# Kernel optimization log

Hardware: AMD Instinct MI355X
Metric: run time of the kernel (lower is better)

The kernel has to match this reference:

```python
import jax, jax.numpy as jnp
import numpy as np

EPS = 1e-5

def _ln(z, g, b):
    # LayerNorm over last axis (per the gammas/betas of shape (2, 3H))
    mu = jnp.mean(z, axis=-1, keepdims=True)
    var = jnp.var(z, axis=-1, keepdims=True)
    return g * (z - mu) * jax.lax.rsqrt(var + EPS) + b

def setup_inputs() -> dict:
    key = jax.random.key(0)
    ks = jax.random.split(key, 12)
    B, L, D_IN, H, A, DEPTH = 64, 512, 256, 256, 128, 4
    glorot = lambda k, sh: jax.random.normal(k, sh, jnp.float32) * np.sqrt(2.0 / (sh[0] + sh[1])).astype(np.float32)
    # variable-length prefix masks (bucketing/masking semantics of the layer)
    lengths = jax.random.randint(ks[0], (B, 1), L // 2, L + 1)
    mask = jnp.arange(L)[None, :] < lengths
    return {
        'x': jax.random.normal(ks[1], (B, L, D_IN), jnp.float32),
        'mask': mask,
        'W_emb': glorot(ks[2], (D_IN, H)),
        'b_emb': jnp.zeros((H,), jnp.float32),
        'W': glorot(ks[3], (H, 3 * H)),
        'U': glorot(ks[4], (H, 3 * H)),
        'b': jnp.zeros((3 * H,), jnp.float32),
        'W_action_1': glorot(ks[5], (H, A)),
        'U_action_1': glorot(ks[6], (H, A)),
        'b_action_1': jnp.zeros((A,), jnp.float32),
        'W_action_2': glorot(ks[7], (A, 2)),
        'b_action_2': jnp.zeros((2,), jnp.float32),
        'gammas': jnp.ones((2, 3 * H), jnp.float32),
        'betas': jnp.zeros((2, 3 * H), jnp.float32),
        'depth': DEPTH,
    }

def _run_depth(x_seq, m_seq, W, U, b, Wa1, Ua1, ba1, Wa2, ba2, gammas, betas):
    # x_seq: (L,B,H), m_seq: (L,B) bool
    H = W.shape[0]
    B = x_seq.shape[1]
    # precompute + layernorm the input projection for all steps (fusable)
    xp_all = _ln(jnp.einsum('lbh,hk->lbk', x_seq, W), gammas[0], betas[0])  # (L,B,3H)

    def step(h, inputs):
        xp, xt, mt = inputs  # (B,3H), (B,H), (B,)
        hp = _ln(h @ U, gammas[1], betas[1])
        r = jax.nn.sigmoid(xp[:, :H] + hp[:, :H] + b[:H])
        z = jax.nn.sigmoid(xp[:, H:2 * H] + hp[:, H:2 * H] + b[H:2 * H])
        hh = jnp.tanh(xp[:, 2 * H:] + r * hp[:, 2 * H:] + b[2 * H:])
        h_new = z * h + (1.0 - z) * hh
        # action-policy subnetwork (binary merge/propagate decision)
        logits = jnp.tanh(xt @ Wa1 + h @ Ua1 + ba1) @ Wa2 + ba2  # (B,2)
        pol = jax.nn.softmax(logits, axis=-1)
        act = (pol[:, 1] > pol[:, 0]) & mt
        h_out = jnp.where(mt[:, None], h_new, h)  # masked steps carry state
        return h_out, (h_out, act, pol)

    h0 = jnp.zeros((B, H), x_seq.dtype)
    _, (h_seq, act_seq, pol_seq) = jax.lax.scan(step, h0, (xp_all, x_seq, m_seq))
    return h_seq, act_seq, pol_seq

def reference(x, mask, W_emb, b_emb, W, U, b, W_action_1, U_action_1, b_action_1,
              W_action_2, b_action_2, gammas, betas, depth):
    # embedding projection, then time-major like the Theano scans
    h_seq = jnp.swapaxes(x @ W_emb + b_emb, 0, 1)  # (L,B,H)
    m_seq = jnp.swapaxes(mask, 0, 1)               # (L,B)
    actions, policies = [], []
    for _ in range(depth):  # vertical (tree-depth) scan: small fixed count
        h_new, act, pol = _run_depth(h_seq, m_seq, W, U, b,
                                     W_action_1, U_action_1, b_action_1,
                                     W_action_2, b_action_2, gammas, betas)
        actions.append(act)
        policies.append(pol)
        h_seq = h_new
        m_seq = m_seq & act  # tree collapse: only selected nodes survive upward
    output = h_seq[-1]  # (B,H) final hidden state of top layer
    action = jnp.stack(actions, 0).transpose(2, 0, 1)      # (B,depth,L)
    policy = jnp.stack(policies, 0).transpose(2, 0, 1, 3)  # (B,depth,L,2)
    return output, action, policy
```

## Files before the change

### kernel.cpp

```cpp
#include <hip/hip_runtime.h>
#include <hip/hip_bf16.h>
#include <math.h>

#define BB 64
#define LL 512
#define HH 256
#define H3 768
#define AA 128
#define NDEPTH 4
#define NROWS (LL*BB)

#define EXCH_U64_PER_CHAIN (2 * 3 * 256)

typedef float vf32x32 __attribute__((ext_vector_type(32)));

__global__ void maskcvt_kernel(const unsigned char* __restrict__ raw,
                               int* __restrict__ m)
{
    int i = blockIdx.x * blockDim.x + threadIdx.x;
    bool bytemode = (raw[1] == 1);
    int v;
    if (bytemode) v = raw[i] ? 1 : 0;
    else          v = (((const int*)raw)[i] != 0) ? 1 : 0;
    m[i] = v;
}

template<int MODE, int EPI>
__global__ __launch_bounds__(256) void gemm_kernel(
    const float* __restrict__ A, const float* __restrict__ Bm,
    const float* __restrict__ bias, const float* __restrict__ aux,
    float* __restrict__ C, int M, int N)
{
    __shared__ float As[16][136];
    __shared__ float Bs[16][136];
    const int tid = threadIdx.x;
    const int tx = tid & 15, ty = tid >> 4;
    const int row0 = blockIdx.y * 128, col0 = blockIdx.x * 128;

    float acc[8][8];
#pragma unroll
    for (int i = 0; i < 8; ++i)
#pragma unroll
        for (int j = 0; j < 8; ++j) acc[i][j] = 0.f;

    for (int kk = 0; kk < 256; kk += 16) {
#pragma unroll
        for (int i = 0; i < 2; ++i) {
            int aid = i * 256 + tid;
            int r   = aid >> 2;
            int k4  = (aid & 3) << 2;
            int rr  = row0 + r;
            float4 v;
            if (MODE == 0) {
                v = *(const float4*)(A + rr * 256 + kk + k4);
            } else if (MODE == 1) {
                v = *(const float4*)(A + (rr & 63) * 131072 + (rr >> 6) * 256 + kk + k4);
            } else {
                if (rr < 64) v = make_float4(0.f, 0.f, 0.f, 0.f);
                else         v = *(const float4*)(A + (rr - 64) * 256 + kk + k4);
            }
            As[k4 + 0][r] = v.x; As[k4 + 1][r] = v.y;
            As[k4 + 2][r] = v.z; As[k4 + 3][r] = v.w;

            int bid = i * 256 + tid;
            int bk  = bid >> 5;
            int c4  = (bid & 31) << 2;
            float4 w = *(const float4*)(Bm + (kk + bk) * N + col0 + c4);
            *(float4*)&Bs[bk][c4] = w;
        }
        __syncthreads();
#pragma unroll
        for (int k = 0; k < 16; ++k) {
            float a[8], bb2[8];
            *(float4*)&a[0]   = *(const float4*)&As[k][ty * 8];
            *(float4*)&a[4]   = *(const float4*)&As[k][ty * 8 + 4];
            *(float4*)&bb2[0] = *(const float4*)&Bs[k][tx * 8];
            *(float4*)&bb2[4] = *(const float4*)&Bs[k][tx * 8 + 4];
#pragma unroll
            for (int i = 0; i < 8; ++i)
#pragma unroll
                for (int j = 0; j < 8; ++j)
                    acc[i][j] += a[i] * bb2[j];
        }
        __syncthreads();
    }

#pragma unroll
    for (int i = 0; i < 8; ++i) {
        int row  = row0 + ty * 8 + i;
        int colb = col0 + tx * 8;
        float vout[8];
#pragma unroll
        for (int j = 0; j < 8; ++j) {
            float v = acc[i][j];
            if (EPI == 1) v += bias[colb + j];
            if (EPI == 2) v = tanhf(v + aux[row * N + colb + j]);
            vout[j] = v;
        }
        *(float4*)&C[row * N + colb]     = *(float4*)&vout[0];
        *(float4*)&C[row * N + colb + 4] = *(float4*)&vout[4];
    }
}

__global__ __launch_bounds__(256) void lnrows_kernel(
    float* __restrict__ XP, const float* __restrict__ g0,
    const float* __restrict__ b0, const float* __restrict__ gb)
{
    const int row = blockIdx.x;
    const int tid = threadIdx.x;
    float* p = XP + (long)row * H3;
    float v0 = p[tid], v1 = p[tid + 256], v2 = p[tid + 512];
    float s = v0 + v1 + v2;
    float q = v0 * v0 + v1 * v1 + v2 * v2;
#pragma unroll
    for (int off = 32; off >= 1; off >>= 1) {
        s += __shfl_xor(s, off);
        q += __shfl_xor(q, off);
    }
    __shared__ float rs4[4], rq4[4];
    if ((tid & 63) == 0) { rs4[tid >> 6] = s; rq4[tid >> 6] = q; }
    __syncthreads();
    float S = rs4[0] + rs4[1] + rs4[2] + rs4[3];
    float Q = rq4[0] + rq4[1] + rq4[2] + rq4[3];
    float mu  = S * (1.f / 768.f);
    float var = Q * (1.f / 768.f) - mu * mu;
    float r   = rsqrtf(var + 1e-5f);
    p[tid]       = g0[tid]       * (v0 - mu) * r + b0[tid]       + gb[tid];
    p[tid + 256] = g0[tid + 256] * (v1 - mu) * r + b0[tid + 256] + gb[tid + 256];
    p[tid + 512] = g0[tid + 512] * (v2 - mu) * r + b0[tid + 512] + gb[tid + 512];
}

__global__ __launch_bounds__(512, 2) void scan3_kernel(
    const float* __restrict__ XP,
    const float* __restrict__ U,
    const float* __restrict__ g1, const float* __restrict__ b1,
    const int* __restrict__ mask,
    float* __restrict__ Y,
    unsigned long long* __restrict__ exch,
    int seq0)
{
    const int i0   = blockIdx.x;
    const int xcd  = i0 & 7;
    const int slot = i0 >> 3;
    const int b    = xcd + 8 * (slot / 3);
    const int s    = slot % 3;
    const int tid  = threadIdx.x;
    const int kg   = tid >> 5;
    const int cg   = tid & 31;
    const int q1   = (s + 1 >= 3) ? s - 2 : s + 1;
    const int q2   = (s + 2 >= 3) ? s - 1 : s + 2;

    __shared__ float h_cur[256];
    __shared__ float part[16][256];
    __shared__ float xp_lds[768];
    __shared__ float g1s[768], b1s[768];
    __shared__ int   mk[512];
    __shared__ float reds[4], redq[4];

    vf32x32 u0v, u1v, u2v, u3v;
    {
        const volatile float* Uv = U;
        const int colbase = s * 256 + cg;
#pragma unroll
        for (int i = 0; i < 16; ++i) {
#pragma unroll
            for (int j = 0; j < 8; ++j) {
                const int f = i * 8 + j;
                float val = Uv[(kg * 16 + i) * H3 + colbase + 32 * j];
                if      (f < 32) u0v[f]      = val;
                else if (f < 64) u1v[f - 32] = val;
                else if (f < 96) u2v[f - 64] = val;
                else             u3v[f - 96] = val;
            }
        }
    }
    if (tid < 256) h_cur[tid] = 0.f;
    for (int i = tid; i < 768; i += 512) { g1s[i] = g1[i]; b1s[i] = b1[i]; }
    mk[tid] = mask[b * LL + tid];
    __syncthreads();

    unsigned long long* exb = exch + b * EXCH_U64_PER_CHAIN;
    int seq = seq0;

    for (int l = 0; l < LL; ++l) {
        if (!mk[l]) {
            if (s == 0 && tid < 64) {
                float4 hv = *(const float4*)&h_cur[tid * 4];
                *(float4*)&Y[((long)l * BB + b) * HH + tid * 4] = hv;
            }
            continue;
        }
        seq++;
        const int par = seq & 1;

        float4 xr4;
        if (tid < 192) xr4 = *(const float4*)(XP + ((long)l * BB + b) * H3 + tid * 4);

        float acc[8] = {0.f, 0.f, 0.f, 0.f, 0.f, 0.f, 0.f, 0.f};
#pragma unroll
        for (int i = 0; i < 4; ++i) {
            float4 hv = *(const float4*)&h_cur[kg * 16 + i * 4];
#pragma unroll
            for (int e = 0; e < 4; ++e) {
                const float hh = (e == 0) ? hv.x : (e == 1) ? hv.y
                               : (e == 2) ? hv.z : hv.w;
                const int ik = i * 4 + e;
#pragma unroll
                for (int j = 0; j < 8; ++j) {
                    const int f = ik * 8 + j;
                    const float uu = (f < 32) ? u0v[f]
                                   : (f < 64) ? u1v[f - 32]
                                   : (f < 96) ? u2v[f - 64]
                                   :            u3v[f - 96];
                    acc[j] += uu * hh;
                }
            }
        }
#pragma unroll
        for (int j = 0; j < 8; ++j)
            part[kg][cg + 32 * j] = acc[j];
        __syncthreads();

        if (tid < 192) *(float4*)&xp_lds[tid * 4] = xr4;

        float pre = 0.f, v0 = 0.f, v1 = 0.f, v2 = 0.f;
        if (tid < 256) {
            pre = part[0][tid];
#pragma unroll
            for (int gg = 1; gg < 16; ++gg) pre += part[gg][tid];

            unsigned long long pk =
                ((unsigned long long)(unsigned)seq << 32) |
                (unsigned long long)__float_as_uint(pre);
            __hip_atomic_store(&exb[(par * 3 + s) * 256 + tid], pk,
                               __ATOMIC_RELAXED, __HIP_MEMORY_SCOPE_AGENT);

            unsigned long long x1, x2;
            do {
                x1 = __hip_atomic_load(&exb[(par * 3 + q1) * 256 + tid],
                                       __ATOMIC_RELAXED, __HIP_MEMORY_SCOPE_AGENT);
            } while ((int)(x1 >> 32) != seq);
            do {
                x2 = __hip_atomic_load(&exb[(par * 3 + q2) * 256 + tid],
                                       __ATOMIC_RELAXED, __HIP_MEMORY_SCOPE_AGENT);
            } while ((int)(x2 >> 32) != seq);
            float w1 = __uint_as_float((unsigned)x1);
            float w2 = __uint_as_float((unsigned)x2);
            v0 = (s == 0) ? pre : ((q1 == 0) ? w1 : w2);
            v1 = (s == 1) ? pre : ((q1 == 1) ? w1 : w2);
            v2 = (s == 2) ? pre : ((q1 == 2) ? w1 : w2);

            float st = v0 + v1 + v2;
            float qt = v0 * v0 + v1 * v1 + v2 * v2;
#pragma unroll
            for (int off = 32; off >= 1; off >>= 1) {
                st += __shfl_xor(st, off);
                qt += __shfl_xor(qt, off);
            }
            if ((tid & 63) == 0) { reds[tid >> 6] = st; redq[tid >> 6] = qt; }
        }
        __syncthreads();

        if (tid < 256) {
            float S = reds[0] + reds[1] + reds[2] + reds[3];
            float Q = redq[0] + redq[1] + redq[2] + redq[3];
            float mu = S * (1.f / 768.f);
            float rs = rsqrtf(Q * (1.f / 768.f) - mu * mu + 1e-5f);
            float hp_r = g1s[tid]       * (v0 - mu) * rs + b1s[tid];
            float hp_z = g1s[256 + tid] * (v1 - mu) * rs + b1s[256 + tid];
            float hp_h = g1s[512 + tid] * (v2 - mu) * rs + b1s[512 + tid];
            float xr = xp_lds[tid], xz = xp_lds[256 + tid], xh = xp_lds[512 + tid];
            float r  = 1.f / (1.f + expf(-(xr + hp_r)));
            float z  = 1.f / (1.f + expf(-(xz + hp_z)));
            float hh = tanhf(xh + r * hp_h);
            float o  = z * h_cur[tid] + (1.f - z) * hh;
            h_cur[tid] = o;
            if (s == 0) Y[((long)l * BB + b) * HH + tid] = o;
        }
        __syncthreads();
    }
}

__global__ __launch_bounds__(256) void act_kernel(
    const float* __restrict__ T, const float* __restrict__ Wa2,
    const float* __restrict__ ba2, const int* __restrict__ mask_in,
    int* __restrict__ mask_out, float* __restrict__ act_out,
    float* __restrict__ pol_out, int d)
{
    int row  = blockIdx.x * 4 + (threadIdx.x >> 6);
    int lane = threadIdx.x & 63;
    const float* Tr = T + (long)row * AA;
    float t0 = Tr[lane], t1 = Tr[lane + 64];
    float l0 = t0 * Wa2[lane * 2]       + t1 * Wa2[(lane + 64) * 2];
    float l1 = t0 * Wa2[lane * 2 + 1]   + t1 * Wa2[(lane + 64) * 2 + 1];
#pragma unroll
    for (int off = 32; off >= 1; off >>= 1) {
        l0 += __shfl_xor(l0, off);
        l1 += __shfl_xor(l1, off);
    }
    if (lane == 0) {
        int l = row >> 6, bb = row & 63;
        l0 += ba2[0]; l1 += ba2[1];
        float m  = fmaxf(l0, l1);
        float e0 = expf(l0 - m), e1 = expf(l1 - m);
        float inv = 1.f / (e0 + e1);
        float p0 = e0 * inv, p1 = e1 * inv;
        int mt = mask_in[bb * LL + l];
        int a  = (p1 > p0) && mt;
        act_out[bb * (NDEPTH * LL) + d * LL + l] = a ? 1.f : 0.f;
        pol_out[bb * (NDEPTH * LL * 2) + d * (LL * 2) + l * 2 + 0] = p0;
        pol_out[bb * (NDEPTH * LL * 2) + d * (LL * 2) + l * 2 + 1] = p1;
        mask_out[bb * LL + l] = a;
    }
}

__global__ void final_copy_kernel(const float* __restrict__ X, float* __restrict__ out)
{
    int i = blockIdx.x * blockDim.x + threadIdx.x;
    int bb = i >> 8, j = i & 255;
    out[i] = X[((long)(LL - 1) * BB + bb) * HH + j];
}

extern "C" void kernel_launch(void* const* d_in, const int* in_sizes, int n_in,
                              void* d_out, int out_size, void* d_ws, size_t ws_size,
                              hipStream_t stream)
{
    const float* x      = (const float*)d_in[0];
    const void*  mraw   = d_in[1];
    const float* W_emb  = (const float*)d_in[2];
    const float* b_emb  = (const float*)d_in[3];
    const float* W      = (const float*)d_in[4];
    const float* U      = (const float*)d_in[5];
    const float* bias3  = (const float*)d_in[6];
    const float* Wa1    = (const float*)d_in[7];
    const float* Ua1    = (const float*)d_in[8];
    const float* ba1    = (const float*)d_in[9];
    const float* Wa2    = (const float*)d_in[10];
    const float* ba2    = (const float*)d_in[11];
    const float* gammas = (const float*)d_in[12];
    const float* betas  = (const float*)d_in[13];

    float* out = (float*)d_out;
    char*  ws  = (char*)d_ws;

    float* XP = (float*)(ws);
    float* X  = (float*)(ws + 100663296UL);
    float* Y  = (float*)(ws + 134217728UL);
    float* XA = (float*)(ws + 167772160UL);
    float* T  = XP;
    int*   m0 = (int*)(ws + 184549376UL);
    int*   m1 = (int*)(ws + 184680448UL);

    float* act_out = out + BB * HH;
    float* pol_out = act_out + BB * NDEPTH * LL;

    maskcvt_kernel<<<dim3(NROWS / 256), dim3(256), 0, stream>>>(
        (const unsigned char*)mraw, m0);

    gemm_kernel<1, 1><<<dim3(2, 256), dim3(256), 0, stream>>>(
        x, W_emb, b_emb, nullptr, X, NROWS, HH);

    float* Xc = X; float* Yc = Y;
    int* mc = m0; int* mn = m1;

    for (int d = 0; d < NDEPTH; ++d) {
        gemm_kernel<0, 0><<<dim3(6, 256), dim3(256), 0, stream>>>(
            Xc, W, nullptr, nullptr, XP, NROWS, H3);
        lnrows_kernel<<<dim3(NROWS), dim3(256), 0, stream>>>(
            XP, gammas, betas, bias3);
        gemm_kernel<0, 1><<<dim3(1, 256), dim3(256), 0, stream>>>(
            Xc, Wa1, ba1, nullptr, XA, NROWS, AA);

        unsigned long long* exch_d = (unsigned long long*)Xc;

        scan3_kernel<<<dim3(192), dim3(512), 0, stream>>>(
            XP, U, gammas + H3, betas + H3, mc, Yc, exch_d, d << 10);

        gemm_kernel<2, 2><<<dim3(1, 256), dim3(256), 0, stream>>>(
            Yc, Ua1, nullptr, XA, T, NROWS, AA);
        act_kernel<<<dim3(NROWS / 4), dim3(256), 0, stream>>>(
            T, Wa2, ba2, mc, mn, act_out, pol_out, d);
        { float* tmp = Xc; Xc = Yc; Yc = tmp; }
        { int* tmp = mc; mc = mn; mn = tmp; }
    }

    final_copy_kernel<<<dim3(BB), dim3(256), 0, stream>>>(Xc, out);
}
```

Measured before the change: 3.663 ms.

## Compact active rows per batch and skip masked rows in input projection and LayerNorm

```diff
diff --git a/kernel.cpp b/kernel.cpp
--- a/kernel.cpp
+++ b/kernel.cpp
@@ -25,17 +25,53 @@
     m[i] = v;
 }
 
+__global__ __launch_bounds__(512) void mkidx_kernel(
+    const int* __restrict__ m,
+    int* __restrict__ rowidx,
+    int* __restrict__ nact)
+{
+    const int b    = blockIdx.x;
+    const int tid  = threadIdx.x;
+    const int lane = tid & 63;
+    const int w    = tid >> 6;
+    __shared__ int wcnt[8];
+    int pred = m[b * LL + tid];
+    unsigned long long bal = __ballot(pred != 0);
+    int below = __popcll(bal & ((1ull << lane) - 1ull));
+    if (lane == 63) wcnt[w] = __popcll(bal);
+    __syncthreads();
+    int woff = 0;
+#pragma unroll
+    for (int i = 0; i < 8; ++i) woff += (i < w) ? wcnt[i] : 0;
+    if (pred) rowidx[b * LL + woff + below] = tid;
+    if (tid == 511) nact[b] = woff + wcnt[7];
+}
+
 template<int MODE, int EPI>
 __global__ __launch_bounds__(256) void gemm_kernel(
     const float* __restrict__ A, const float* __restrict__ Bm,
     const float* __restrict__ bias, const float* __restrict__ aux,
-    float* __restrict__ C, int M, int N)
+    float* __restrict__ C, int M, int N,
+    const int* __restrict__ ridx, const int* __restrict__ nact)
 {
     __shared__ float As[16][136];
     __shared__ float Bs[16][136];
     const int tid = threadIdx.x;
     const int tx = tid & 15, ty = tid >> 4;
     const int row0 = blockIdx.y * 128, col0 = blockIdx.x * 128;
+
+    int arow0 = 0, arow1 = 0;
+    if (MODE == 3) {
+        const int bb = row0 >> 9;
+        const int na = nact[bb];
+        if ((row0 & 511) >= na) return;
+        const int r0 = row0 + (tid >> 2);
+        const int r1 = r0 + 64;
+        const int l0 = ((r0 & 511) < na) ? ridx[r0] : 0;
+        const int l1 = ((r1 & 511) < na) ? ridx[r1] : 0;
+        arow0 = l0 * 64 + bb;
+        arow1 = l1 * 64 + bb;
+    }
 
     float acc[8][8];
 #pragma unroll
@@ -55,9 +91,12 @@
                 v = *(const float4*)(A + rr * 256 + kk + k4);
             } else if (MODE == 1) {
                 v = *(const float4*)(A + (rr & 63) * 131072 + (rr >> 6) * 256 + kk + k4);
-            } else {
+            } else if (MODE == 2) {
                 if (rr < 64) v = make_float4(0.f, 0.f, 0.f, 0.f);
                 else         v = *(const float4*)(A + (rr - 64) * 256 + kk + k4);
+            } else {
+                int ar = i ? arow1 : arow0;
+                v = *(const float4*)(A + ar * 256 + kk + k4);
             }
             As[k4 + 0][r] = v.x; As[k4 + 1][r] = v.y;
             As[k4 + 2][r] = v.z; As[k4 + 3][r] = v.w;
@@ -104,9 +143,11 @@
 
 __global__ __launch_bounds__(256) void lnrows_kernel(
     float* __restrict__ XP, const float* __restrict__ g0,
-    const float* __restrict__ b0, const float* __restrict__ gb)
+    const float* __restrict__ b0, const float* __restrict__ gb,
+    const int* __restrict__ nact)
 {
     const int row = blockIdx.x;
+    if ((row & 511) >= nact[row >> 9]) return;
     const int tid = threadIdx.x;
     float* p = XP + (long)row * H3;
     float v0 = p[tid], v1 = p[tid + 256], v2 = p[tid + 512];
@@ -192,9 +233,10 @@
         }
         seq++;
         const int par = seq & 1;
+        const int cs  = seq - seq0 - 1;
 
         float4 xr4;
-        if (tid < 192) xr4 = *(const float4*)(XP + ((long)l * BB + b) * H3 + tid * 4);
+        if (tid < 192) xr4 = *(const float4*)(XP + ((long)(b * LL + cs)) * H3 + tid * 4);
 
         float acc[8] = {0.f, 0.f, 0.f, 0.f, 0.f, 0.f, 0.f, 0.f};
 #pragma unroll
@@ -235,15 +277,18 @@
             __hip_atomic_store(&exb[(par * 3 + s) * 256 + tid], pk,
                                __ATOMIC_RELAXED, __HIP_MEMORY_SCOPE_AGENT);
 
-            unsigned long long x1, x2;
+            unsigned long long x1 = 0, x2 = 0;
+            bool d1 = false, d2 = false;
             do {
-                x1 = __hip_atomic_load(&exb[(par * 3 + q1) * 256 + tid],
-                                       __ATOMIC_RELAXED, __HIP_MEMORY_SCOPE_AGENT);
-            } while ((int)(x1 >> 32) != seq);
-            do {
-                x2 = __hip_atomic_load(&exb[(par * 3 + q2) * 256 + tid],
-                                       __ATOMIC_RELAXED, __HIP_MEMORY_SCOPE_AGENT);
-            } while ((int)(x2 >> 32) != seq);
+                unsigned long long t1 =
+                    __hip_atomic_load(&exb[(par * 3 + q1) * 256 + tid],
+                                      __ATOMIC_RELAXED, __HIP_MEMORY_SCOPE_AGENT);
+                unsigned long long t2 =
+                    __hip_atomic_load(&exb[(par * 3 + q2) * 256 + tid],
+                                      __ATOMIC_RELAXED, __HIP_MEMORY_SCOPE_AGENT);
+                if (!d1 && (int)(t1 >> 32) == seq) { x1 = t1; d1 = true; }
+                if (!d2 && (int)(t2 >> 32) == seq) { x2 = t2; d2 = true; }
+            } while (!(d1 && d2));
             float w1 = __uint_as_float((unsigned)x1);
             float w2 = __uint_as_float((unsigned)x2);
             v0 = (s == 0) ? pre : ((q1 == 0) ? w1 : w2);
@@ -358,18 +403,24 @@
         (const unsigned char*)mraw, m0);
 
     gemm_kernel<1, 1><<<dim3(2, 256), dim3(256), 0, stream>>>(
-        x, W_emb, b_emb, nullptr, X, NROWS, HH);
+        x, W_emb, b_emb, nullptr, X, NROWS, HH, nullptr, nullptr);
 
     float* Xc = X; float* Yc = Y;
     int* mc = m0; int* mn = m1;
 
     for (int d = 0; d < NDEPTH; ++d) {
-        gemm_kernel<0, 0><<<dim3(6, 256), dim3(256), 0, stream>>>(
-            Xc, W, nullptr, nullptr, XP, NROWS, H3);
+        int* rowidx = (int*)Yc;
+        int* nactp  = ((int*)Yc) + NROWS;
+
+        mkidx_kernel<<<dim3(BB), dim3(512), 0, stream>>>(mc, rowidx, nactp);
+
+        gemm_kernel<3, 0><<<dim3(6, 256), dim3(256), 0, stream>>>(
+            Xc, W, nullptr, nullptr, XP, NROWS, H3, rowidx, nactp);
         lnrows_kernel<<<dim3(NROWS), dim3(256), 0, stream>>>(
-            XP, gammas, betas, bias3);
+            XP, gammas, betas, bias3, nactp);
+
         gemm_kernel<0, 1><<<dim3(1, 256), dim3(256), 0, stream>>>(
-            Xc, Wa1, ba1, nullptr, XA, NROWS, AA);
+            Xc, Wa1, ba1, nullptr, XA, NROWS, AA, nullptr, nullptr);
 
         unsigned long long* exch_d = (unsigned long long*)Xc;
 
@@ -377,7 +428,7 @@
             XP, U, gammas + H3, betas + H3, mc, Yc, exch_d, d << 10);
 
         gemm_kernel<2, 2><<<dim3(1, 256), dim3(256), 0, stream>>>(
-            Yc, Ua1, nullptr, XA, T, NROWS, AA);
+            Yc, Ua1, nullptr, XA, T, NROWS, AA, nullptr, nullptr);
         act_kernel<<<dim3(NROWS / 4), dim3(256), 0, stream>>>(
             T, Wa2, ba2, mc, mn, act_out, pol_out, d);
         { float* tmp = Xc; Xc = Yc; Yc = tmp; }
```

Result: faster. 3.398 ms (-7.2%).
